# Performance work log

Measured on AMD Instinct MI355X. Metric: run time of the kernel, lower is better.

The kernel has to match this reference:

```python
import jax, jax.numpy as jnp
import numpy as np

K = 3  # kernel_size

def setup_inputs() -> dict:
    key = jax.random.key(0)
    k1, k2, k3 = jax.random.split(key, 3)
    B, C, H, W = 8, 64, 128, 128
    x = jax.random.normal(k1, (B, C, H, W), dtype=jnp.float32)
    # 1x1 conv weight (out_channels*K*K, in_channels) and bias
    W_gen = jax.random.normal(k2, (C * K * K, C), dtype=jnp.float32) / np.float32(np.sqrt(C))
    b_gen = jax.random.normal(k3, (C * K * K,), dtype=jnp.float32) * 0.01
    return {"x": x, "W_gen": W_gen, "b_gen": b_gen}

def reference(x, W_gen, b_gen):
    B, C, H, W = x.shape  # out_channels == in_channels (required by the view)
    # filter_gen: 1x1 conv + ReLU -> (B, C*K*K, H, W)
    f = jax.nn.relu(jnp.einsum('bchw,oc->bohw', x, W_gen) + b_gen[None, :, None, None])
    filters = f.reshape(B, C, K * K, H, W)
    # F.unfold with padding=(K-1)//2, stride 1: gather KxK patches per pixel.
    pad = (K - 1) // 2
    xp = jnp.pad(x, ((0, 0), (0, 0), (pad, pad), (pad, pad)))
    # kernel-position index runs row-major (i*K + j), matching unfold layout
    patches = jnp.stack([xp[:, :, i:i + H, j:j + W]
                         for i in range(K) for j in range(K)], axis=2)  # (B,C,K*K,H,W)
    out = (filters * patches).sum(axis=2)  # (B,C,H,W)
    return out
```

## Files before the change

kernel.cpp:

```cpp
#include <hip/hip_runtime.h>
#include <hip/hip_bf16.h>

#define CC 64
#define HH 128
#define WW 128
#define OO 576
#define HW (HH * WW)

typedef __attribute__((ext_vector_type(8))) short short8;
typedef __attribute__((ext_vector_type(4))) float floatx4;

__device__ __forceinline__ unsigned short f2bf(float f) {
    unsigned u = __float_as_uint(f);
    u = (u + 0x7FFFu + ((u >> 16) & 1u)) >> 16;
    return (unsigned short)u;
}

__global__ void ACDA_wconv_kernel(const float* __restrict__ Wg,
                                  unsigned short* __restrict__ Wb) {
    int i = blockIdx.x * 256 + threadIdx.x;
    if (i < OO * CC) Wb[i] = f2bf(Wg[i]);
}

__global__ __launch_bounds__(256, 4) void ACDA_main_kernel(
    const float* __restrict__ x, const unsigned short* __restrict__ Wb,
    const float* __restrict__ bg, float* __restrict__ out)
{
    __shared__ float FbufT[4][64][20];

    const int tid  = threadIdx.x;
    const int lane = tid & 63;
    const int wv   = tid >> 6;
    const int quad = lane >> 4;
    const int l16  = lane & 15;

    const int bid = blockIdx.x;
    const int wk  = (bid & 7) * 256 + (bid >> 3);
    const int seg = wk & 1;
    const int h   = (wk >> 1) & 127;
    const int b   = wk >> 8;
    const int w0  = seg << 6;

    const float* xb = x + (size_t)b * CC * HW;

    short8 bfrag[4][2];
#pragma unroll
    for (int nt = 0; nt < 4; ++nt) {
#pragma unroll
        for (int ks = 0; ks < 2; ++ks) {
            short8 v;
            const int w = w0 + nt * 16 + l16;
#pragma unroll
            for (int j = 0; j < 8; j += 2) {
                const int c = ks * 32 + quad * 8 + j;
                float f0 = xb[(c * HH + h) * WW + w];
                float f1 = xb[((c + 1) * HH + h) * WW + w];
                __hip_bfloat162 p = __float22bfloat162_rn(make_float2(f0, f1));
                unsigned u;
                __builtin_memcpy(&u, &p, 4);
                v[j]     = (short)(u & 0xffffu);
                v[j + 1] = (short)(u >> 16);
            }
            bfrag[nt][ks] = v;
        }
    }

    int wA = w0 + lane - 1; bool badA = (wA < 0);   if (badA) wA = 0;
    int wB = w0 + lane;
    int wC = w0 + lane + 1; bool badC = (wC > 127); if (badC) wC = 127;
    int rt[3]; bool rbad[3];
#pragma unroll
    for (int di = 0; di < 3; ++di) {
        int rr = h + di - 1;
        rbad[di] = (rr < 0) || (rr > 127);
        rr = rr < 0 ? 0 : (rr > 127 ? 127 : rr);
        rt[di] = rr * WW;
    }
    const int wsel[3]  = {wA, wB, wC};
    const bool wbad[3] = {badA, false, badC};
    const int soffC = wv * 16 * HW;
    int  pb[3][3]; bool bad[3][3];
#pragma unroll
    for (int di = 0; di < 3; ++di)
#pragma unroll
        for (int dj = 0; dj < 3; ++dj) {
            pb[di][dj]  = soffC + rt[di] + wsel[dj];
            bad[di][dj] = rbad[di] || wbad[dj];
        }

    float oacc[16];
#pragma unroll
    for (int i = 0; i < 16; ++i) oacc[i] = 0.f;

#pragma unroll
    for (int t = 0; t < 9; ++t) {
        const int obase = wv * 144 + t * 16;
        const unsigned short* wrow = Wb + (obase + l16) * CC + quad * 8;
        short8 a0 = *(const short8*)(wrow);
        short8 a1 = *(const short8*)(wrow + 32);
#pragma unroll
        for (int nt = 0; nt < 4; ++nt) {
            floatx4 z = {0.f, 0.f, 0.f, 0.f};
            z = __builtin_amdgcn_mfma_f32_16x16x32_bf16(a0, bfrag[nt][0], z, 0, 0, 0);
            z = __builtin_amdgcn_mfma_f32_16x16x32_bf16(a1, bfrag[nt][1], z, 0, 0, 0);
            *(floatx4*)&FbufT[wv][nt * 16 + l16][quad * 4] = z;
        }

#pragma unroll
        for (int g = 0; g < 4; ++g) {
            floatx4 f4 = *(const floatx4*)&FbufT[wv][lane][g * 4];
#pragma unroll
            for (int rr = 0; rr < 4; ++rr) {
                const int r     = g * 4 + rr;
                const int idx   = t * 16 + r;
                const int c_rel = idx / 9;
                const int kk    = idx - 9 * c_rel;
                const int di    = kk / 3;
                const int dj    = kk - 3 * di;
                float fv = f4[rr] + bg[obase + r];
                fv = fmaxf(fv, 0.f);
                float pv = xb[pb[di][dj] + c_rel * HW];
                if (bad[di][dj]) pv = 0.f;
                oacc[c_rel] = fmaf(fv, pv, oacc[c_rel]);
            }
        }
    }

    float* ob = out + (size_t)b * CC * HW + h * WW + w0 + lane;
#pragma unroll
    for (int i = 0; i < 16; ++i)
        ob[(wv * 16 + i) * HW] = oacc[i];
}

extern "C" void kernel_launch(void* const* d_in, const int* in_sizes, int n_in,
                              void* d_out, int out_size, void* d_ws, size_t ws_size,
                              hipStream_t stream) {
    const float* x  = (const float*)d_in[0];
    const float* Wg = (const float*)d_in[1];
    const float* bg = (const float*)d_in[2];
    float* out = (float*)d_out;
    unsigned short* Wb = (unsigned short*)d_ws;

    ACDA_wconv_kernel<<<dim3((OO * CC + 255) / 256), dim3(256), 0, stream>>>(Wg, Wb);
    ACDA_main_kernel<<<dim3(8 * 128 * 2), dim3(256), 0, stream>>>(x, Wb, bg, out);
}
```

Measured before the change: 118.6 us.

## Software-pipeline weight and patch loads across filter chunks, fold bias into MFMA

Restructures the 9-chunk loop into a double-buffered pipeline: the weight fragments, bias and the 16 patch values for chunk t+1 are loaded into registers while chunk t runs its MFMAs and FMAs. Bias is now loaded as a vector and used as the MFMA accumulator init, so the scalar bias add per element goes away. The occupancy hint in launch bounds is dropped to make room for the larger register footprint. The risk is lower occupancy and more register pressure, which weakens latency hiding across waves.

```diff
diff --git a/kernel.cpp b/kernel.cpp
--- a/kernel.cpp
+++ b/kernel.cpp
@@ -22,7 +22,7 @@
     if (i < OO * CC) Wb[i] = f2bf(Wg[i]);
 }
 
-__global__ __launch_bounds__(256, 4) void ACDA_main_kernel(
+__global__ __launch_bounds__(256) void ACDA_main_kernel(
     const float* __restrict__ x, const unsigned short* __restrict__ Wb,
     const float* __restrict__ bg, float* __restrict__ out)
 {
@@ -42,28 +42,6 @@
     const int w0  = seg << 6;
 
     const float* xb = x + (size_t)b * CC * HW;
-
-    short8 bfrag[4][2];
-#pragma unroll
-    for (int nt = 0; nt < 4; ++nt) {
-#pragma unroll
-        for (int ks = 0; ks < 2; ++ks) {
-            short8 v;
-            const int w = w0 + nt * 16 + l16;
-#pragma unroll
-            for (int j = 0; j < 8; j += 2) {
-                const int c = ks * 32 + quad * 8 + j;
-                float f0 = xb[(c * HH + h) * WW + w];
-                float f1 = xb[((c + 1) * HH + h) * WW + w];
-                __hip_bfloat162 p = __float22bfloat162_rn(make_float2(f0, f1));
-                unsigned u;
-                __builtin_memcpy(&u, &p, 4);
-                v[j]     = (short)(u & 0xffffu);
-                v[j + 1] = (short)(u >> 16);
-            }
-            bfrag[nt][ks] = v;
-        }
-    }
 
     int wA = w0 + lane - 1; bool badA = (wA < 0);   if (badA) wA = 0;
     int wB = w0 + lane;
@@ -88,43 +66,99 @@
             bad[di][dj] = rbad[di] || wbad[dj];
         }
 
+    short8 bfrag[4][2];
+#pragma unroll
+    for (int nt = 0; nt < 4; ++nt) {
+#pragma unroll
+        for (int ks = 0; ks < 2; ++ks) {
+            short8 v;
+            const int w = w0 + nt * 16 + l16;
+#pragma unroll
+            for (int j = 0; j < 8; j += 2) {
+                const int c = ks * 32 + quad * 8 + j;
+                float f0 = xb[(c * HH + h) * WW + w];
+                float f1 = xb[((c + 1) * HH + h) * WW + w];
+                __hip_bfloat162 p = __float22bfloat162_rn(make_float2(f0, f1));
+                unsigned u;
+                __builtin_memcpy(&u, &p, 4);
+                v[j]     = (short)(u & 0xffffu);
+                v[j + 1] = (short)(u >> 16);
+            }
+            bfrag[nt][ks] = v;
+        }
+    }
+
     float oacc[16];
 #pragma unroll
     for (int i = 0; i < 16; ++i) oacc[i] = 0.f;
 
-#pragma unroll
-    for (int t = 0; t < 9; ++t) {
-        const int obase = wv * 144 + t * 16;
-        const unsigned short* wrow = Wb + (obase + l16) * CC + quad * 8;
-        short8 a0 = *(const short8*)(wrow);
-        short8 a1 = *(const short8*)(wrow + 32);
-#pragma unroll
-        for (int nt = 0; nt < 4; ++nt) {
-            floatx4 z = {0.f, 0.f, 0.f, 0.f};
-            z = __builtin_amdgcn_mfma_f32_16x16x32_bf16(a0, bfrag[nt][0], z, 0, 0, 0);
-            z = __builtin_amdgcn_mfma_f32_16x16x32_bf16(a1, bfrag[nt][1], z, 0, 0, 0);
-            *(floatx4*)&FbufT[wv][nt * 16 + l16][quad * 4] = z;
-        }
+    short8 a0A, a1A, a0B, a1B;
+    floatx4 bvA, bvB;
+    float pvA[16], pvB[16];
 
-#pragma unroll
-        for (int g = 0; g < 4; ++g) {
-            floatx4 f4 = *(const floatx4*)&FbufT[wv][lane][g * 4];
-#pragma unroll
-            for (int rr = 0; rr < 4; ++rr) {
-                const int r     = g * 4 + rr;
-                const int idx   = t * 16 + r;
-                const int c_rel = idx / 9;
-                const int kk    = idx - 9 * c_rel;
-                const int di    = kk / 3;
-                const int dj    = kk - 3 * di;
-                float fv = f4[rr] + bg[obase + r];
-                fv = fmaxf(fv, 0.f);
-                float pv = xb[pb[di][dj] + c_rel * HW];
-                if (bad[di][dj]) pv = 0.f;
-                oacc[c_rel] = fmaf(fv, pv, oacc[c_rel]);
-            }
-        }
-    }
+#define LOADA(T, A0, A1, BV) do {                                         \
+        const int obase_ = wv * 144 + (T) * 16;                           \
+        const unsigned short* wrow_ = Wb + (obase_ + l16) * CC + quad * 8;\
+        (A0) = *(const short8*)(wrow_);                                   \
+        (A1) = *(const short8*)(wrow_ + 32);                              \
+        (BV) = *(const floatx4*)(bg + obase_ + quad * 4);                 \
+    } while (0)
+
+#define LOADP(T, PV) do {                                                 \
+        _Pragma("unroll")                                                 \
+        for (int r_ = 0; r_ < 16; ++r_) {                                 \
+            const int idx_ = (T) * 16 + r_;                               \
+            const int c_   = idx_ / 9;                                    \
+            const int kk_  = idx_ - 9 * c_;                               \
+            const int di_  = kk_ / 3;                                     \
+            const int dj_  = kk_ - 3 * di_;                               \
+            float v_ = xb[pb[di_][dj_] + c_ * HW];                        \
+            (PV)[r_] = bad[di_][dj_] ? 0.f : v_;                          \
+        }                                                                 \
+    } while (0)
+
+    LOADA(0, a0A, a1A, bvA);
+    LOADP(0, pvA);
+
+#define CHUNK(T, PVC, PVN, A0C, A1C, BVC, A0N, A1N, BVN) do {             \
+        _Pragma("unroll")                                                 \
+        for (int nt_ = 0; nt_ < 4; ++nt_) {                               \
+            floatx4 z_ = (BVC);    \
+            z_ = __builtin_amdgcn_mfma_f32_16x16x32_bf16((A0C), bfrag[nt_][0], z_, 0, 0, 0); \
+            z_ = __builtin_amdgcn_mfma_f32_16x16x32_bf16((A1C), bfrag[nt_][1], z_, 0, 0, 0); \
+            *(floatx4*)&FbufT[wv][nt_ * 16 + l16][quad * 4] = z_;         \
+        }                                                                 \
+        if ((T) < 8) {                                                    \
+            LOADA((T) + 1, A0N, A1N, BVN);                                \
+            LOADP((T) + 1, PVN);                                          \
+        }                                                                 \
+        _Pragma("unroll")                                                 \
+        for (int g_ = 0; g_ < 4; ++g_) {                                  \
+            floatx4 f4_ = *(const floatx4*)&FbufT[wv][lane][g_ * 4];      \
+            _Pragma("unroll")                                             \
+            for (int rr_ = 0; rr_ < 4; ++rr_) {                           \
+                const int r_   = g_ * 4 + rr_;                            \
+                const int idx_ = (T) * 16 + r_;                           \
+                const int c_   = idx_ / 9;                                \
+                float fv_ = fmaxf(f4_[rr_], 0.f);                         \
+                oacc[c_] = fmaf(fv_, (PVC)[r_], oacc[c_]);                \
+            }                                                             \
+        }                                                                 \
+    } while (0)
+
+    CHUNK(0, pvA, pvB, a0A, a1A, bvA, a0B, a1B, bvB);
+    CHUNK(1, pvB, pvA, a0B, a1B, bvB, a0A, a1A, bvA);
+    CHUNK(2, pvA, pvB, a0A, a1A, bvA, a0B, a1B, bvB);
+    CHUNK(3, pvB, pvA, a0B, a1B, bvB, a0A, a1A, bvA);
+    CHUNK(4, pvA, pvB, a0A, a1A, bvA, a0B, a1B, bvB);
+    CHUNK(5, pvB, pvA, a0B, a1B, bvB, a0A, a1A, bvA);
+    CHUNK(6, pvA, pvB, a0A, a1A, bvA, a0B, a1B, bvB);
+    CHUNK(7, pvB, pvA, a0B, a1B, bvB, a0A, a1A, bvA);
+    CHUNK(8, pvA, pvB, a0A, a1A, bvA, a0B, a1B, bvB);
+
+#undef CHUNK
+#undef LOADP
+#undef LOADA
 
     float* ob = out + (size_t)b * CC * HW + h * WW + w0 + lane;
 #pragma unroll
```

Measured after the change: 116.8 us. No clear change (-1.6%).

## Permute filter weights by tap and stage input halo tile in shared memory

Applied to the files above, without the earlier changes.

The prep kernel reorders the generator weights and bias so that output rows are grouped by kernel tap (kk*64 + c). MFMA output rows then map directly to channels, which lets the ReLU and multiply-accumulate run straight on the MFMA accumulators instead of round-tripping through an LDS transpose buffer. The input 3-row halo tile is staged once into shared memory in a channel-contiguous layout. The B fragments and all nine patch taps are read from there instead of through scattered per-element global loads. This adds a block-level barrier and a larger LDS footprint, which may reduce occupancy.

```diff
diff --git a/kernel.cpp b/kernel.cpp
--- a/kernel.cpp
+++ b/kernel.cpp
@@ -17,22 +17,35 @@
 }
 
 __global__ void ACDA_wconv_kernel(const float* __restrict__ Wg,
-                                  unsigned short* __restrict__ Wb) {
+                                  const float* __restrict__ bg,
+                                  unsigned short* __restrict__ Wb,
+                                  float* __restrict__ Bp) {
     int i = blockIdx.x * 256 + threadIdx.x;
-    if (i < OO * CC) Wb[i] = f2bf(Wg[i]);
+    if (i < OO * CC) {
+        int o2  = i >> 6;
+        int col = i & 63;
+        int kk  = o2 >> 6;
+        int c   = o2 & 63;
+        Wb[i] = f2bf(Wg[(c * 9 + kk) * CC + col]);
+    }
+    if (i < OO) {
+        Bp[i] = bg[(i & 63) * 9 + (i >> 6)];
+    }
 }
 
 __global__ __launch_bounds__(256, 4) void ACDA_main_kernel(
     const float* __restrict__ x, const unsigned short* __restrict__ Wb,
-    const float* __restrict__ bg, float* __restrict__ out)
+    const float* __restrict__ Bp, float* __restrict__ out)
 {
-    __shared__ float FbufT[4][64][20];
+    __shared__ float S[3][66][68];
+    float* Sf = &S[0][0][0];
 
     const int tid  = threadIdx.x;
     const int lane = tid & 63;
     const int wv   = tid >> 6;
     const int quad = lane >> 4;
     const int l16  = lane & 15;
+    const int c0   = wv * 16;
 
     const int bid = blockIdx.x;
     const int wk  = (bid & 7) * 256 + (bid >> 3);
@@ -43,93 +56,96 @@
 
     const float* xb = x + (size_t)b * CC * HW;
 
+#pragma unroll
+    for (int di = 0; di < 3; ++di) {
+        const int hh = h + di - 1;
+        const bool oob = (hh < 0) || (hh > 127);
+        const int hc = hh < 0 ? 0 : (hh > 127 ? 127 : hh);
+        const float* src = xb + hc * WW + w0 + lane;
+#pragma unroll
+        for (int i2 = 0; i2 < 4; ++i2) {
+            const int c = c0 + 4 * i2;
+            floatx4 v;
+            if (!oob) {
+                v[0] = src[(c + 0) * HW]; v[1] = src[(c + 1) * HW];
+                v[2] = src[(c + 2) * HW]; v[3] = src[(c + 3) * HW];
+            } else {
+                v = floatx4{0.f, 0.f, 0.f, 0.f};
+            }
+            *(floatx4*)&Sf[(di * 66 + lane + 1) * 68 + c] = v;
+        }
+    }
+    if (tid < 192) {
+        const int di = tid >> 6, c = tid & 63;
+        const int hh = h + di - 1;
+        const bool oobR = (hh < 0) || (hh > 127);
+        const int hc = hh < 0 ? 0 : (hh > 127 ? 127 : hh);
+        float vL = 0.f, vR = 0.f;
+        if (!oobR) {
+            if (w0 > 0)        vL = xb[c * HW + hc * WW + w0 - 1];
+            if (w0 + 64 < WW)  vR = xb[c * HW + hc * WW + w0 + 64];
+        }
+        Sf[(di * 66 + 0)  * 68 + c] = vL;
+        Sf[(di * 66 + 65) * 68 + c] = vR;
+    }
+    __syncthreads();
+
     short8 bfrag[4][2];
 #pragma unroll
-    for (int nt = 0; nt < 4; ++nt) {
+    for (int nt = 0; nt < 4; ++nt)
 #pragma unroll
         for (int ks = 0; ks < 2; ++ks) {
+            const float* p = &Sf[(66 + nt * 16 + l16 + 1) * 68 + ks * 32 + quad * 8];
+            floatx4 f0 = *(const floatx4*)p;
+            floatx4 f1 = *(const floatx4*)(p + 4);
             short8 v;
-            const int w = w0 + nt * 16 + l16;
+            __hip_bfloat162 p0 = __float22bfloat162_rn(make_float2(f0[0], f0[1]));
+            __hip_bfloat162 p1 = __float22bfloat162_rn(make_float2(f0[2], f0[3]));
+            __hip_bfloat162 p2 = __float22bfloat162_rn(make_float2(f1[0], f1[1]));
+            __hip_bfloat162 p3 = __float22bfloat162_rn(make_float2(f1[2], f1[3]));
+            unsigned u0, u1, u2, u3;
+            __builtin_memcpy(&u0, &p0, 4); __builtin_memcpy(&u1, &p1, 4);
+            __builtin_memcpy(&u2, &p2, 4); __builtin_memcpy(&u3, &p3, 4);
+            v[0] = (short)(u0 & 0xffffu); v[1] = (short)(u0 >> 16);
+            v[2] = (short)(u1 & 0xffffu); v[3] = (short)(u1 >> 16);
+            v[4] = (short)(u2 & 0xffffu); v[5] = (short)(u2 >> 16);
+            v[6] = (short)(u3 & 0xffffu); v[7] = (short)(u3 >> 16);
+            bfrag[nt][ks] = v;
+        }
+
+    floatx4 acc[4];
 #pragma unroll
-            for (int j = 0; j < 8; j += 2) {
-                const int c = ks * 32 + quad * 8 + j;
-                float f0 = xb[(c * HH + h) * WW + w];
-                float f1 = xb[((c + 1) * HH + h) * WW + w];
-                __hip_bfloat162 p = __float22bfloat162_rn(make_float2(f0, f1));
-                unsigned u;
-                __builtin_memcpy(&u, &p, 4);
-                v[j]     = (short)(u & 0xffffu);
-                v[j + 1] = (short)(u >> 16);
-            }
-            bfrag[nt][ks] = v;
+    for (int nt = 0; nt < 4; ++nt) acc[nt] = floatx4{0.f, 0.f, 0.f, 0.f};
+
+#pragma unroll
+    for (int t = 0; t < 9; ++t) {
+        const int di = t / 3;
+        const int dj = t - 3 * di;
+        const unsigned short* wrow = Wb + (t * 64 + c0 + l16) * CC + quad * 8;
+        short8 a0 = *(const short8*)(wrow);
+        short8 a1 = *(const short8*)(wrow + 32);
+        floatx4 bv = *(const floatx4*)(Bp + t * 64 + c0 + 4 * quad);
+        floatx4 pv[4];
+#pragma unroll
+        for (int nt = 0; nt < 4; ++nt)
+            pv[nt] = *(const floatx4*)&Sf[(di * 66 + nt * 16 + l16 + dj) * 68 + c0 + 4 * quad];
+#pragma unroll
+        for (int nt = 0; nt < 4; ++nt) {
+            floatx4 z = bv;
+            z = __builtin_amdgcn_mfma_f32_16x16x32_bf16(a0, bfrag[nt][0], z, 0, 0, 0);
+            z = __builtin_amdgcn_mfma_f32_16x16x32_bf16(a1, bfrag[nt][1], z, 0, 0, 0);
+#pragma unroll
+            for (int rg = 0; rg < 4; ++rg)
+                acc[nt][rg] = fmaf(fmaxf(z[rg], 0.f), pv[nt][rg], acc[nt][rg]);
         }
     }
 
-    int wA = w0 + lane - 1; bool badA = (wA < 0);   if (badA) wA = 0;
-    int wB = w0 + lane;
-    int wC = w0 + lane + 1; bool badC = (wC > 127); if (badC) wC = 127;
-    int rt[3]; bool rbad[3];
+    float* ob = out + (size_t)b * CC * HW + h * WW + w0;
 #pragma unroll
-    for (int di = 0; di < 3; ++di) {
-        int rr = h + di - 1;
-        rbad[di] = (rr < 0) || (rr > 127);
-        rr = rr < 0 ? 0 : (rr > 127 ? 127 : rr);
-        rt[di] = rr * WW;
-    }
-    const int wsel[3]  = {wA, wB, wC};
-    const bool wbad[3] = {badA, false, badC};
-    const int soffC = wv * 16 * HW;
-    int  pb[3][3]; bool bad[3][3];
+    for (int nt = 0; nt < 4; ++nt)
 #pragma unroll
-    for (int di = 0; di < 3; ++di)
-#pragma unroll
-        for (int dj = 0; dj < 3; ++dj) {
-            pb[di][dj]  = soffC + rt[di] + wsel[dj];
-            bad[di][dj] = rbad[di] || wbad[dj];
-        }
-
-    float oacc[16];
-#pragma unroll
-    for (int i = 0; i < 16; ++i) oacc[i] = 0.f;
-
-#pragma unroll
-    for (int t = 0; t < 9; ++t) {
-        const int obase = wv * 144 + t * 16;
-        const unsigned short* wrow = Wb + (obase + l16) * CC + quad * 8;
-        short8 a0 = *(const short8*)(wrow);
-        short8 a1 = *(const short8*)(wrow + 32);
-#pragma unroll
-        for (int nt = 0; nt < 4; ++nt) {
-            floatx4 z = {0.f, 0.f, 0.f, 0.f};
-            z = __builtin_amdgcn_mfma_f32_16x16x32_bf16(a0, bfrag[nt][0], z, 0, 0, 0);
-            z = __builtin_amdgcn_mfma_f32_16x16x32_bf16(a1, bfrag[nt][1], z, 0, 0, 0);
-            *(floatx4*)&FbufT[wv][nt * 16 + l16][quad * 4] = z;
-        }
-
-#pragma unroll
-        for (int g = 0; g < 4; ++g) {
-            floatx4 f4 = *(const floatx4*)&FbufT[wv][lane][g * 4];
-#pragma unroll
-            for (int rr = 0; rr < 4; ++rr) {
-                const int r     = g * 4 + rr;
-                const int idx   = t * 16 + r;
-                const int c_rel = idx / 9;
-                const int kk    = idx - 9 * c_rel;
-                const int di    = kk / 3;
-                const int dj    = kk - 3 * di;
-                float fv = f4[rr] + bg[obase + r];
-                fv = fmaxf(fv, 0.f);
-                float pv = xb[pb[di][dj] + c_rel * HW];
-                if (bad[di][dj]) pv = 0.f;
-                oacc[c_rel] = fmaf(fv, pv, oacc[c_rel]);
-            }
-        }
-    }
-
-    float* ob = out + (size_t)b * CC * HW + h * WW + w0 + lane;
-#pragma unroll
-    for (int i = 0; i < 16; ++i)
-        ob[(wv * 16 + i) * HW] = oacc[i];
+        for (int rg = 0; rg < 4; ++rg)
+            ob[(c0 + 4 * quad + rg) * HW + nt * 16 + l16] = acc[nt][rg];
 }
 
 extern "C" void kernel_launch(void* const* d_in, const int* in_sizes, int n_in,
@@ -140,7 +156,8 @@
     const float* bg = (const float*)d_in[2];
     float* out = (float*)d_out;
     unsigned short* Wb = (unsigned short*)d_ws;
+    float* Bp = (float*)((char*)d_ws + OO * CC * 2);
 
-    ACDA_wconv_kernel<<<dim3((OO * CC + 255) / 256), dim3(256), 0, stream>>>(Wg, Wb);
-    ACDA_main_kernel<<<dim3(8 * 128 * 2), dim3(256), 0, stream>>>(x, Wb, bg, out);
+    ACDA_wconv_kernel<<<dim3((OO * CC + 255) / 256), dim3(256), 0, stream>>>(Wg, bg, Wb, Bp);
+    ACDA_main_kernel<<<dim3(8 * 128 * 2), dim3(256), 0, stream>>>(x, Wb, Bp, out);
 }
```

Measured after the change: 110.7 us. -6.7%, faster.
